# Optimization experiments

Hardware: AMD Instinct MI355X
Metric: run time of the kernel (lower is better)

## Reference

```python
import jax, jax.numpy as jnp
import numpy as np

VOCAB = 33
D = 256
B = 64
L = 4096


def setup_inputs() -> dict:
    key = jax.random.key(0)
    ks = jax.random.split(key, 7)
    X = jax.random.randint(ks[0], (B, L), 0, VOCAB, dtype=jnp.int64)
    valid_lens = jax.random.randint(ks[1], (B,), 0, L, dtype=jnp.int64)
    emb = jax.random.normal(ks[2], (VOCAB, D), dtype=jnp.float32)
    W1 = jax.random.normal(ks[3], (D, D), dtype=jnp.float32) * (1.0 / np.sqrt(D))
    b1 = jnp.zeros((D,), dtype=jnp.float32)
    W2 = jax.random.normal(ks[4], (D, D), dtype=jnp.float32) * (1.0 / np.sqrt(D))
    b2 = jnp.zeros((D,), dtype=jnp.float32)
    return {"X": X, "valid_lens": valid_lens, "emb": emb, "W1": W1, "b1": b1, "W2": W2, "b2": b2}


def reference(X, valid_lens, emb, W1, b1, W2, b2):
    # Embedding gather: [B, L, D]
    e = emb[X]
    # Length mask (on-device, no python loop): positions >= valid_len zeroed
    mask = (jnp.arange(L)[None, :] < valid_lens[:, None]).astype(e.dtype)  # [B, L]
    # Masked sum-pool over sequence -> [B, D]
    pooled = jnp.einsum("bld,bl->bd", e, mask)
    # Two-layer MLP with ReLU (dropout is identity in eval)
    h = jax.nn.relu(pooled @ W1 + b1)
    out = jax.nn.relu(h @ W2 + b2)
    return out
```

## Files before the change

kernel.cpp:

```cpp
#include <hip/hip_runtime.h>

#define B_SZ  64
#define L_SZ  4096
#define VOCAB 33
#define D_SZ  256
#define NT    512
#define NW    8
#define G     8
#define KPG   32
#define C     64

__global__ __launch_bounds__(NT) void prot_net_fused(
    const int* __restrict__ X,
    const int* __restrict__ valid_lens,
    const float* __restrict__ emb,
    const float* __restrict__ W1,
    const float* __restrict__ b1,
    const float* __restrict__ W2,
    const float* __restrict__ b2,
    float* __restrict__ out)
{
    __shared__ int    s_cnt[NW][VOCAB];
    __shared__ float4 s_part[G][C];
    __shared__ float  s_vec[D_SZ];

    const int b   = blockIdx.x;
    const int tid = threadIdx.x;
    const int g   = tid >> 6;
    const int c   = tid & 63;

    const float4* emb4 = reinterpret_cast<const float4*>(emb);
    const float4* W14  = reinterpret_cast<const float4*>(W1);
    const float4* W24  = reinterpret_cast<const float4*>(W2);

    float4 e4[4];
    #pragma unroll
    for (int j = 0; j < 4; ++j)
        e4[j] = emb4[(g * 4 + j) * C + c];
    float4 e32 = make_float4(0.f, 0.f, 0.f, 0.f);
    if (g == 0) e32 = emb4[32 * C + c];

    float4 bias1 = make_float4(0.f, 0.f, 0.f, 0.f);
    float4 bias2 = make_float4(0.f, 0.f, 0.f, 0.f);
    if (tid < C) {
        bias1 = reinterpret_cast<const float4*>(b1)[tid];
        bias2 = reinterpret_cast<const float4*>(b2)[tid];
    }
    const int   vl    = valid_lens[b];
    const int4* xrow4 = reinterpret_cast<const int4*>(X + (size_t)b * L_SZ);
    const int4  t0    = xrow4[tid];
    const int4  t1    = xrow4[tid + NT];

    if (tid < NW * VOCAB) ((int*)s_cnt)[tid] = 0;
    __syncthreads();

    const int l0 = tid * 4;
    const int l1 = (tid + NT) * 4;
    if (l0 + 0 < vl) atomicAdd(&s_cnt[g][t0.x], 1);
    if (l0 + 1 < vl) atomicAdd(&s_cnt[g][t0.y], 1);
    if (l0 + 2 < vl) atomicAdd(&s_cnt[g][t0.z], 1);
    if (l0 + 3 < vl) atomicAdd(&s_cnt[g][t0.w], 1);
    if (l1 + 0 < vl) atomicAdd(&s_cnt[g][t1.x], 1);
    if (l1 + 1 < vl) atomicAdd(&s_cnt[g][t1.y], 1);
    if (l1 + 2 < vl) atomicAdd(&s_cnt[g][t1.z], 1);
    if (l1 + 3 < vl) atomicAdd(&s_cnt[g][t1.w], 1);
    __syncthreads();

    float cf[4];
    #pragma unroll
    for (int j = 0; j < 4; ++j) {
        int s = 0;
        #pragma unroll
        for (int w = 0; w < NW; ++w) s += s_cnt[w][g * 4 + j];
        cf[j] = (float)s;
    }
    float c32 = 0.f;
    if (g == 0) {
        int s = 0;
        #pragma unroll
        for (int w = 0; w < NW; ++w) s += s_cnt[w][32];
        c32 = (float)s;
    }

    float4 p = make_float4(0.f, 0.f, 0.f, 0.f);
    #pragma unroll
    for (int j = 0; j < 4; ++j) {
        p.x = fmaf(cf[j], e4[j].x, p.x);
        p.y = fmaf(cf[j], e4[j].y, p.y);
        p.z = fmaf(cf[j], e4[j].z, p.z);
        p.w = fmaf(cf[j], e4[j].w, p.w);
    }
    p.x = fmaf(c32, e32.x, p.x);
    p.y = fmaf(c32, e32.y, p.y);
    p.z = fmaf(c32, e32.z, p.z);
    p.w = fmaf(c32, e32.w, p.w);
    s_part[g][c] = p;
    __syncthreads();

    if (tid < C) {
        float4 s = s_part[0][tid];
        #pragma unroll
        for (int g2 = 1; g2 < G; ++g2) {
            float4 q = s_part[g2][tid];
            s.x += q.x; s.y += q.y; s.z += q.z; s.w += q.w;
        }
        reinterpret_cast<float4*>(s_vec)[tid] = s;
    }
    __syncthreads();

    float4 acc = make_float4(0.f, 0.f, 0.f, 0.f);
    #pragma unroll
    for (int j = 0; j < KPG; ++j) {
        int k = g * KPG + j;
        float  sv = s_vec[k];
        float4 w  = W14[k * C + c];
        acc.x = fmaf(sv, w.x, acc.x);
        acc.y = fmaf(sv, w.y, acc.y);
        acc.z = fmaf(sv, w.z, acc.z);
        acc.w = fmaf(sv, w.w, acc.w);
    }
    s_part[g][c] = acc;
    __syncthreads();

    if (tid < C) {
        float4 h = bias1;
        #pragma unroll
        for (int g2 = 0; g2 < G; ++g2) {
            float4 q = s_part[g2][tid];
            h.x += q.x; h.y += q.y; h.z += q.z; h.w += q.w;
        }
        h.x = fmaxf(h.x, 0.f); h.y = fmaxf(h.y, 0.f);
        h.z = fmaxf(h.z, 0.f); h.w = fmaxf(h.w, 0.f);
        reinterpret_cast<float4*>(s_vec)[tid] = h;
    }
    __syncthreads();

    float4 acc2 = make_float4(0.f, 0.f, 0.f, 0.f);
    #pragma unroll
    for (int j = 0; j < KPG; ++j) {
        int k = g * KPG + j;
        float  sv = s_vec[k];
        float4 w  = W24[k * C + c];
        acc2.x = fmaf(sv, w.x, acc2.x);
        acc2.y = fmaf(sv, w.y, acc2.y);
        acc2.z = fmaf(sv, w.z, acc2.z);
        acc2.w = fmaf(sv, w.w, acc2.w);
    }
    s_part[g][c] = acc2;
    __syncthreads();

    if (tid < C) {
        float4 o = bias2;
        #pragma unroll
        for (int g2 = 0; g2 < G; ++g2) {
            float4 q = s_part[g2][tid];
            o.x += q.x; o.y += q.y; o.z += q.z; o.w += q.w;
        }
        o.x = fmaxf(o.x, 0.f); o.y = fmaxf(o.y, 0.f);
        o.z = fmaxf(o.z, 0.f); o.w = fmaxf(o.w, 0.f);
        reinterpret_cast<float4*>(out + (size_t)b * D_SZ)[tid] = o;
    }
}

extern "C" void kernel_launch(void* const* d_in, const int* in_sizes, int n_in,
                              void* d_out, int out_size, void* d_ws, size_t ws_size,
                              hipStream_t stream) {
    const int*   X          = (const int*)d_in[0];
    const int*   valid_lens = (const int*)d_in[1];
    const float* emb        = (const float*)d_in[2];
    const float* W1         = (const float*)d_in[3];
    const float* b1         = (const float*)d_in[4];
    const float* W2         = (const float*)d_in[5];
    const float* b2         = (const float*)d_in[6];
    float* out = (float*)d_out;

    prot_net_fused<<<B_SZ, NT, 0, stream>>>(X, valid_lens, emb, W1, b1, W2, b2, out);
}
```

Measured before the change: 11.47 us.

## Split each batch row across four blocks by output column group and prefetch W2

Launches four blocks per batch row so there are 256 blocks instead of 64, which fills more compute units on the GPU. Each block recomputes the histogram, pooling and the full first layer, then computes only its 64-column slice of the second layer. The block's W2 slice is prefetched into registers at kernel start, so the load latency overlaps the histogram phase. The cost is redundant work: the X row reads, the histogram and the W1 matvec are each done four times, and register pressure rises.

```diff
diff --git a/kernel.cpp b/kernel.cpp
--- a/kernel.cpp
+++ b/kernel.cpp
@@ -6,11 +6,9 @@
 #define D_SZ  256
 #define NT    512
 #define NW    8
-#define G     8
-#define KPG   32
 #define C     64
 
-__global__ __launch_bounds__(NT) void prot_net_fused(
+__global__ __launch_bounds__(NT) void prot_fused(
     const int* __restrict__ X,
     const int* __restrict__ valid_lens,
     const float* __restrict__ emb,
@@ -21,17 +19,23 @@
     float* __restrict__ out)
 {
     __shared__ int    s_cnt[NW][VOCAB];
-    __shared__ float4 s_part[G][C];
+    __shared__ float4 s_part[NW][C];
     __shared__ float  s_vec[D_SZ];
 
-    const int b   = blockIdx.x;
-    const int tid = threadIdx.x;
-    const int g   = tid >> 6;
-    const int c   = tid & 63;
+    const int bid = blockIdx.x;
+    const int b   = bid >> 2;
+    const int cg  = bid & 3;
+    const int t   = threadIdx.x;
+    const int g   = t >> 6;
+    const int c   = t & 63;
 
     const float4* emb4 = reinterpret_cast<const float4*>(emb);
     const float4* W14  = reinterpret_cast<const float4*>(W1);
-    const float4* W24  = reinterpret_cast<const float4*>(W2);
+
+    float w2[32];
+    #pragma unroll
+    for (int q = 0; q < 32; ++q)
+        w2[q] = W2[(g * 32 + q) * D_SZ + cg * 64 + c];
 
     float4 e4[4];
     #pragma unroll
@@ -41,21 +45,19 @@
     if (g == 0) e32 = emb4[32 * C + c];
 
     float4 bias1 = make_float4(0.f, 0.f, 0.f, 0.f);
-    float4 bias2 = make_float4(0.f, 0.f, 0.f, 0.f);
-    if (tid < C) {
-        bias1 = reinterpret_cast<const float4*>(b1)[tid];
-        bias2 = reinterpret_cast<const float4*>(b2)[tid];
-    }
+    if (t < C) bias1 = reinterpret_cast<const float4*>(b1)[t];
+    const float bias2 = (t < 64) ? b2[cg * 64 + t] : 0.f;
+
     const int   vl    = valid_lens[b];
     const int4* xrow4 = reinterpret_cast<const int4*>(X + (size_t)b * L_SZ);
-    const int4  t0    = xrow4[tid];
-    const int4  t1    = xrow4[tid + NT];
+    const int4  t0    = xrow4[t];
+    const int4  t1    = xrow4[t + NT];
 
-    if (tid < NW * VOCAB) ((int*)s_cnt)[tid] = 0;
+    if (t < NW * VOCAB) ((int*)s_cnt)[t] = 0;
     __syncthreads();
 
-    const int l0 = tid * 4;
-    const int l1 = (tid + NT) * 4;
+    const int l0 = t * 4;
+    const int l1 = (t + NT) * 4;
     if (l0 + 0 < vl) atomicAdd(&s_cnt[g][t0.x], 1);
     if (l0 + 1 < vl) atomicAdd(&s_cnt[g][t0.y], 1);
     if (l0 + 2 < vl) atomicAdd(&s_cnt[g][t0.z], 1);
@@ -97,23 +99,23 @@
     s_part[g][c] = p;
     __syncthreads();
 
-    if (tid < C) {
-        float4 s = s_part[0][tid];
+    if (t < C) {
+        float4 s = s_part[0][t];
         #pragma unroll
-        for (int g2 = 1; g2 < G; ++g2) {
-            float4 q = s_part[g2][tid];
+        for (int g2 = 1; g2 < NW; ++g2) {
+            float4 q = s_part[g2][t];
             s.x += q.x; s.y += q.y; s.z += q.z; s.w += q.w;
         }
-        reinterpret_cast<float4*>(s_vec)[tid] = s;
+        reinterpret_cast<float4*>(s_vec)[t] = s;
     }
     __syncthreads();
 
     float4 acc = make_float4(0.f, 0.f, 0.f, 0.f);
     #pragma unroll
-    for (int j = 0; j < KPG; ++j) {
-        int k = g * KPG + j;
-        float  sv = s_vec[k];
-        float4 w  = W14[k * C + c];
+    for (int j = 0; j < 32; ++j) {
+        const int   k  = g * 32 + j;
+        const float sv = s_vec[k];
+        const float4 w = W14[k * C + c];
         acc.x = fmaf(sv, w.x, acc.x);
         acc.y = fmaf(sv, w.y, acc.y);
         acc.z = fmaf(sv, w.z, acc.z);
@@ -122,43 +124,31 @@
     s_part[g][c] = acc;
     __syncthreads();
 
-    if (tid < C) {
+    if (t < C) {
         float4 h = bias1;
         #pragma unroll
-        for (int g2 = 0; g2 < G; ++g2) {
-            float4 q = s_part[g2][tid];
+        for (int g2 = 0; g2 < NW; ++g2) {
+            float4 q = s_part[g2][t];
             h.x += q.x; h.y += q.y; h.z += q.z; h.w += q.w;
         }
         h.x = fmaxf(h.x, 0.f); h.y = fmaxf(h.y, 0.f);
         h.z = fmaxf(h.z, 0.f); h.w = fmaxf(h.w, 0.f);
-        reinterpret_cast<float4*>(s_vec)[tid] = h;
+        reinterpret_cast<float4*>(s_vec)[t] = h;
     }
     __syncthreads();
 
-    float4 acc2 = make_float4(0.f, 0.f, 0.f, 0.f);
+    float acc2 = 0.f;
     #pragma unroll
-    for (int j = 0; j < KPG; ++j) {
-        int k = g * KPG + j;
-        float  sv = s_vec[k];
-        float4 w  = W24[k * C + c];
-        acc2.x = fmaf(sv, w.x, acc2.x);
-        acc2.y = fmaf(sv, w.y, acc2.y);
-        acc2.z = fmaf(sv, w.z, acc2.z);
-        acc2.w = fmaf(sv, w.w, acc2.w);
-    }
-    s_part[g][c] = acc2;
+    for (int q = 0; q < 32; ++q)
+        acc2 = fmaf(s_vec[g * 32 + q], w2[q], acc2);
+    ((float*)s_part)[g * 64 + c] = acc2;
     __syncthreads();
 
-    if (tid < C) {
-        float4 o = bias2;
+    if (t < 64) {
+        float o = bias2;
         #pragma unroll
-        for (int g2 = 0; g2 < G; ++g2) {
-            float4 q = s_part[g2][tid];
-            o.x += q.x; o.y += q.y; o.z += q.z; o.w += q.w;
-        }
-        o.x = fmaxf(o.x, 0.f); o.y = fmaxf(o.y, 0.f);
-        o.z = fmaxf(o.z, 0.f); o.w = fmaxf(o.w, 0.f);
-        reinterpret_cast<float4*>(out + (size_t)b * D_SZ)[tid] = o;
+        for (int q = 0; q < NW; ++q) o += ((float*)s_part)[q * 64 + t];
+        out[(size_t)b * D_SZ + cg * 64 + t] = fmaxf(o, 0.f);
     }
 }
 
@@ -174,5 +164,5 @@
     const float* b2         = (const float*)d_in[6];
     float* out = (float*)d_out;
 
-    prot_net_fused<<<B_SZ, NT, 0, stream>>>(X, valid_lens, emb, W1, b1, W2, b2, out);
+    prot_fused<<<256, NT, 0, stream>>>(X, valid_lens, emb, W1, b1, W2, b2, out);
 }
```

Measured after the change: 10.96 us. 4.5% less time.
